# Performance work log

Hardware: AMD Instinct MI355X
Metric: run time of the kernel (lower is better)

The kernel has to match this reference:

```python
import jax, jax.numpy as jnp
import numpy as np

NF = 10      # num RBF / Chebyshev features
GAMMA = 1.0
EMB = 10
H = 64
NHEADS = 2


def _rbf(d):
    centers = jnp.arange(1, NF + 1, dtype=d.dtype)
    return jnp.exp(-GAMMA * (centers - d[..., None]) ** 2)


def _cheb(a):
    feats = [jnp.ones_like(a), a]
    for _ in range(2, NF):
        feats.append(2 * a * feats[-1] - feats[-2])
    return jnp.stack(feats, -1)


def _gru_layer(xs, wih, whh, bih, bhh):
    # xs: [L, B, D] -> [L, B, H]; PyTorch gate order r, z, n
    B = xs.shape[1]
    def step(h, xt):
        gi = xt @ wih.T + bih
        gh = h @ whh.T + bhh
        ir, iz, inn = jnp.split(gi, 3, -1)
        hr, hz, hn = jnp.split(gh, 3, -1)
        r = jax.nn.sigmoid(ir + hr)
        z = jax.nn.sigmoid(iz + hz)
        n = jnp.tanh(inn + r * hn)
        hnew = (1 - z) * n + z * h
        return hnew, hnew
    h0 = jnp.zeros((B, H), xs.dtype)
    _, ys = jax.lax.scan(step, h0, xs)
    return ys


def _mha(x, in_w, in_b, out_w, out_b):
    B, L, E = x.shape
    hd = E // NHEADS
    qkv = x @ in_w.T + in_b
    q, k, v = jnp.split(qkv, 3, -1)
    sp = lambda t: t.reshape(B, L, NHEADS, hd).transpose(0, 2, 1, 3)
    q, k, v = sp(q), sp(k), sp(v)
    scale = 1.0 / float(np.sqrt(hd))
    att = jax.nn.softmax(jnp.einsum('bhqd,bhkd->bhqk', q, k) * scale, -1)
    o = jnp.einsum('bhqk,bhkd->bhqd', att, v).transpose(0, 2, 1, 3).reshape(B, L, E)
    return o @ out_w.T + out_b


def _ln(x, s, b):
    m = x.mean(-1, keepdims=True)
    v = ((x - m) ** 2).mean(-1, keepdims=True)
    return (x - m) / jnp.sqrt(v + 1e-5) * s + b


def setup_inputs() -> dict:
    key = jax.random.key(0)
    ks = jax.random.split(key, 48)
    N, L = 384, 256
    # bond rows: [atom_idx1, atom_idx2, bond_dist]; angle rows: [d1, d2, angle]
    idx1 = jax.random.randint(ks[0], (N, L), 1, 119).astype(jnp.float32)
    idx2 = jax.random.randint(ks[1], (N, L), 1, 119).astype(jnp.float32)
    dist = jax.random.uniform(ks[2], (N, L), minval=0.5, maxval=5.0)
    d1 = jax.random.uniform(ks[3], (N, L), minval=0.5, maxval=5.0)
    d2 = jax.random.uniform(ks[4], (N, L), minval=0.5, maxval=5.0)
    ang = jax.random.uniform(ks[5], (N, L), minval=-1.0, maxval=1.0)
    bond_x = jnp.stack([idx1, idx2, dist], 1)
    angle_x = jnp.stack([d1, d2, ang], 1)
    is_angle = (jnp.arange(N) % 3 == 2)
    x = jnp.where(is_angle[:, None, None], angle_x, bond_x)

    def nrm(k, shp, s=0.1):
        return jax.random.normal(k, shp) * s

    D_IN = 2 * EMB + NF  # 30
    inp = {
        'x': x,
        'emb': nrm(ks[6], (119, EMB), 1.0),
        'wih0': nrm(ks[7], (3 * H, D_IN)),
        'whh0': nrm(ks[8], (3 * H, H)),
        'bih0': nrm(ks[9], (3 * H,)),
        'bhh0': nrm(ks[10], (3 * H,)),
        'wih12': nrm(ks[11], (2, 3 * H, H)),
        'whh12': nrm(ks[12], (2, 3 * H, H)),
        'bih12': nrm(ks[13], (2, 3 * H)),
        'bhh12': nrm(ks[14], (2, 3 * H)),
        'in_w1': nrm(ks[15], (3 * H, H)),
        'in_b1': nrm(ks[16], (3 * H,)),
        'out_w1': nrm(ks[17], (H, H)),
        'out_b1': nrm(ks[18], (H,)),
        'in_w2': nrm(ks[19], (3 * H, H)),
        'in_b2': nrm(ks[20], (3 * H,)),
        'out_w2': nrm(ks[21], (H, H)),
        'out_b2': nrm(ks[22], (H,)),
        'ff_w1': nrm(ks[23], (1024, H)),
        'ff_b1': nrm(ks[24], (1024,)),
        'ff_w2': nrm(ks[25], (H, 1024)),
        'ff_b2': nrm(ks[26], (H,)),
        'ln1_s': jnp.ones((H,)), 'ln1_b': jnp.zeros((H,)),
        'ln2_s': jnp.ones((H,)), 'ln2_b': jnp.zeros((H,)),
        'ln3_s': jnp.ones((H,)), 'ln3_b': jnp.zeros((H,)),
        'ln4_s': jnp.ones((H,)), 'ln4_b': jnp.zeros((H,)),
        'fw1': nrm(ks[27], (256, H)), 'fb1': nrm(ks[28], (256,)),
        'fw2': nrm(ks[29], (64, 256)), 'fb2': nrm(ks[30], (64,)),
        'fw3': nrm(ks[31], (32, 64)), 'fb3': nrm(ks[32], (32,)),
        'fw4': nrm(ks[33], (1, 32)), 'fb4': nrm(ks[34], (1,)),
    }
    return inp


def reference(x, emb, wih0, whh0, bih0, bhh0, wih12, whh12, bih12, bhh12,
              in_w1, in_b1, out_w1, out_b1, in_w2, in_b2, out_w2, out_b2,
              ff_w1, ff_b1, ff_w2, ff_b2,
              ln1_s, ln1_b, ln2_s, ln2_b, ln3_s, ln3_b, ln4_s, ln4_b,
              fw1, fb1, fw2, fb2, fw3, fb3, fw4, fb4):
    # Vectorized featurization (replaces the per-triplet Python loop):
    # rows with i%3 in {0,1} are bond rows, i%3==2 are angle rows.
    i1 = jnp.clip(x[:, 0].astype(jnp.int32), 0, 118)
    i2 = jnp.clip(x[:, 1].astype(jnp.int32), 0, 118)
    bond_feat = jnp.concatenate([emb[i1], emb[i2], _rbf(x[:, 2])], -1)
    angle_feat = jnp.concatenate([_rbf(x[:, 0]), _rbf(x[:, 1]), _cheb(x[:, 2])], -1)
    is_angle = (jnp.arange(x.shape[0]) % 3 == 2)
    feat = jnp.where(is_angle[:, None, None], angle_feat, bond_feat)  # [N, L, 30]

    hs = feat.transpose(1, 0, 2)  # [L, N, 30]
    hs = _gru_layer(hs, wih0, whh0, bih0, bhh0)
    for l in range(2):
        hs = _gru_layer(hs, wih12[l], whh12[l], bih12[l], bhh12[l])
    g = hs.transpose(1, 0, 2)  # [N, L, H]

    def ffn(t):
        return jax.nn.relu(jax.nn.relu(t @ ff_w1.T + ff_b1) @ ff_w2.T + ff_b2)

    a = _mha(g, in_w1, in_b1, out_w1, out_b1)
    h = _ln(g + a, ln1_s, ln1_b)
    h = _ln(h + ffn(h), ln2_s, ln2_b)
    a = _mha(h, in_w2, in_b2, out_w2, out_b2)
    h = _ln(a + a, ln3_s, ln3_b)  # faithful to original: attn_out + attn_out
    h = _ln(h + ffn(h), ln4_s, ln4_b)
    o = h[:, -1, :]
    o = jax.nn.silu(o @ fw1.T + fb1)
    o = jax.nn.silu(o @ fw2.T + fb2)
    o = jax.nn.silu(o @ fw3.T + fb3)
    o = o @ fw4.T + fb4
    return o.squeeze(-1)
```

## Files before the change

### kernel.cpp

```cpp
#include <hip/hip_runtime.h>

static constexpr int NB   = 384;
static constexpr int SEQL = 256;
static constexpr int NROWS = NB * SEQL;

typedef short bf16x8 __attribute__((ext_vector_type(8)));
typedef float f32x4  __attribute__((ext_vector_type(4)));

union B8u {
    bf16x8 v;
    ushort us[8];
    uint4  q;
};

__device__ inline ushort f2bf(float f) {
    uint u = __float_as_uint(f);
    uint r = u + 0x7FFFu + ((u >> 16) & 1u);
    return (ushort)(r >> 16);
}

__device__ inline void split8(float4 a, float4 b, B8u& hi, B8u& lo) {
    float f[8] = {a.x, a.y, a.z, a.w, b.x, b.y, b.z, b.w};
    #pragma unroll
    for (int i = 0; i < 8; ++i) {
        ushort h = f2bf(f[i]);
        hi.us[i] = h;
        float fh = __uint_as_float(((uint)h) << 16);
        lo.us[i] = f2bf(f[i] - fh);
    }
}

__global__ __launch_bounds__(256) void split_kernel(
    const float* __restrict__ src, ushort* __restrict__ hi,
    ushort* __restrict__ lo, int n)
{
    int i = blockIdx.x * 256 + threadIdx.x;
    if (i < n) {
        float f = src[i];
        ushort h = f2bf(f);
        hi[i] = h;
        float fh = __uint_as_float(((uint)h) << 16);
        lo[i] = f2bf(f - fh);
    }
}

__global__ __launch_bounds__(192) void featproj_kernel(
    const float* __restrict__ x, const float* __restrict__ emb,
    const float* __restrict__ wih0, const float* __restrict__ bih0,
    float* __restrict__ X)
{
    __shared__ float F[32][33];
    const int tid = threadIdx.x;
    const int m0  = blockIdx.x * 32;

    if (tid < 96) {
        const int r   = tid & 31;
        const int grp = tid >> 5;
        const int m   = m0 + r;
        const int b   = m % NB;
        const int l   = m / NB;
        const float* xb = x + (size_t)b * (3 * SEQL);
        const float x0 = xb[l], x1 = xb[SEQL + l], x2 = xb[2 * SEQL + l];
        const bool is_angle = (b % 3) == 2;
        float o[10];
        if (is_angle) {
            if (grp < 2) {
                const float a = (grp == 0) ? x0 : x1;
                #pragma unroll
                for (int c = 0; c < 10; ++c) { float d = (float)(c + 1) - a; o[c] = __expf(-d * d); }
            } else {
                float t0 = 1.f, t1 = x2;
                o[0] = 1.f; o[1] = x2;
                #pragma unroll
                for (int c = 2; c < 10; ++c) { float t = 2.f * x2 * t1 - t0; o[c] = t; t0 = t1; t1 = t; }
            }
        } else {
            if (grp < 2) {
                const float xv = (grp == 0) ? x0 : x1;
                int idx = (int)xv; idx = idx < 0 ? 0 : (idx > 118 ? 118 : idx);
                #pragma unroll
                for (int c = 0; c < 10; ++c) o[c] = emb[idx * 10 + c];
            } else {
                #pragma unroll
                for (int c = 0; c < 10; ++c) { float d = (float)(c + 1) - x2; o[c] = __expf(-d * d); }
            }
        }
        #pragma unroll
        for (int c = 0; c < 10; ++c) F[r][grp * 10 + c] = o[c];
    }
    __syncthreads();

    float w[30];
    #pragma unroll
    for (int k = 0; k < 30; ++k) w[k] = wih0[tid * 30 + k];
    const float bj = bih0[tid];
    for (int r = 0; r < 32; ++r) {
        float acc = bj;
        #pragma unroll
        for (int k = 0; k < 30; ++k) acc += F[r][k] * w[k];
        X[(size_t)(m0 + r) * 192 + tid] = acc;
    }
}

__global__ __launch_bounds__(192) void gru_kernel(
    const float* __restrict__ X, const float* __restrict__ whh,
    const float* __restrict__ bhh, float* __restrict__ Y, int out_batch_major)
{
    const int b = blockIdx.x;
    const int j = threadIdx.x;
    __shared__ float h[64];
    __shared__ float gis[192], ghs[192];

    float w[64];
    #pragma unroll
    for (int k = 0; k < 64; ++k) w[k] = whh[j * 64 + k];
    const float bj = bhh[j];
    if (j < 64) h[j] = 0.f;
    __syncthreads();

    for (int t = 0; t < SEQL; ++t) {
        const float gi = X[((size_t)t * NB + b) * 192 + j];
        float gh = bj;
        #pragma unroll
        for (int k = 0; k < 64; ++k) gh += h[k] * w[k];
        gis[j] = gi; ghs[j] = gh;
        __syncthreads();
        if (j < 64) {
            const float r = 1.f / (1.f + __expf(-(gis[j] + ghs[j])));
            const float z = 1.f / (1.f + __expf(-(gis[64 + j] + ghs[64 + j])));
            const float n = tanhf(gis[128 + j] + r * ghs[128 + j]);
            const float hn = (1.f - z) * n + z * h[j];
            h[j] = hn;
            const size_t row = out_batch_major ? ((size_t)b * SEQL + t)
                                               : ((size_t)t * NB + b);
            Y[row * 64 + j] = hn;
        }
        __syncthreads();
    }
}

template<int NCOLS>
__global__ __launch_bounds__(256, 2) void gemm_mfma(
    const float* __restrict__ A, const ushort* __restrict__ Whi,
    const ushort* __restrict__ Wlo, const float* __restrict__ bias,
    float* __restrict__ C)
{
    const int tid = threadIdx.x;
    const int w   = tid >> 6;
    const int lane = tid & 63;
    const int c = lane & 15;
    const int g = lane >> 4;
    const int m0 = blockIdx.x * 128 + 32 * w;

    B8u ah[2][2], al[2][2];
    #pragma unroll
    for (int rm = 0; rm < 2; ++rm) {
        const float* ap = A + (size_t)(m0 + 16 * rm + c) * 64;
        #pragma unroll
        for (int ks = 0; ks < 2; ++ks) {
            float4 v0 = *(const float4*)(ap + 32 * ks + 8 * g);
            float4 v1 = *(const float4*)(ap + 32 * ks + 8 * g + 4);
            split8(v0, v1, ah[rm][ks], al[rm][ks]);
        }
    }

    f32x4 acc[NCOLS / 16][2];
    #pragma unroll
    for (int nt = 0; nt < NCOLS / 16; ++nt) {
        float bv = bias[16 * nt + c];
        #pragma unroll
        for (int rm = 0; rm < 2; ++rm)
            acc[nt][rm] = (f32x4){bv, bv, bv, bv};
    }

    #pragma unroll
    for (int nt = 0; nt < NCOLS / 16; ++nt) {
        B8u wh[2], wl[2];
        #pragma unroll
        for (int ks = 0; ks < 2; ++ks) {
            size_t off = (size_t)(16 * nt + c) * 64 + 32 * ks + 8 * g;
            wh[ks].q = *(const uint4*)(Whi + off);
            wl[ks].q = *(const uint4*)(Wlo + off);
        }
        #pragma unroll
        for (int rm = 0; rm < 2; ++rm)
            #pragma unroll
            for (int ks = 0; ks < 2; ++ks) {
                acc[nt][rm] = __builtin_amdgcn_mfma_f32_16x16x32_bf16(ah[rm][ks].v, wh[ks].v, acc[nt][rm], 0, 0, 0);
                acc[nt][rm] = __builtin_amdgcn_mfma_f32_16x16x32_bf16(al[rm][ks].v, wh[ks].v, acc[nt][rm], 0, 0, 0);
                acc[nt][rm] = __builtin_amdgcn_mfma_f32_16x16x32_bf16(ah[rm][ks].v, wl[ks].v, acc[nt][rm], 0, 0, 0);
            }
    }

    #pragma unroll
    for (int nt = 0; nt < NCOLS / 16; ++nt)
        #pragma unroll
        for (int rm = 0; rm < 2; ++rm)
            #pragma unroll
            for (int reg = 0; reg < 4; ++reg) {
                int row = m0 + 16 * rm + 4 * g + reg;
                C[(size_t)row * NCOLS + 16 * nt + reg * 0 + c] = acc[nt][rm][reg];
            }
}

__global__ __launch_bounds__(256, 2) void ffn_mfma(
    const float* __restrict__ Xin,
    const ushort* __restrict__ W1hi, const ushort* __restrict__ W1lo,
    const ushort* __restrict__ W2hi, const ushort* __restrict__ W2lo,
    const float* __restrict__ b1, const float* __restrict__ b2,
    float* __restrict__ Out)
{
    __shared__ __align__(16) ushort sW1h[64 * 72], sW1l[64 * 72];
    __shared__ __align__(16) ushort sW2h[64 * 72], sW2l[64 * 72];
    __shared__ __align__(16) ushort sHh[128 * 72], sHl[128 * 72];
    __shared__ float sb1[64];

    const int tid = threadIdx.x;
    const int w   = tid >> 6;
    const int lane = tid & 63;
    const int c = lane & 15;
    const int g = lane >> 4;
    const int r0 = blockIdx.x * 128;

    B8u xh[2][2], xl[2][2];
    #pragma unroll
    for (int rm = 0; rm < 2; ++rm) {
        const float* ap = Xin + (size_t)(r0 + 32 * w + 16 * rm + c) * 64;
        #pragma unroll
        for (int ks = 0; ks < 2; ++ks) {
            float4 v0 = *(const float4*)(ap + 32 * ks + 8 * g);
            float4 v1 = *(const float4*)(ap + 32 * ks + 8 * g + 4);
            split8(v0, v1, xh[rm][ks], xl[rm][ks]);
        }
    }

    f32x4 acc2[4][2];
    #pragma unroll
    for (int jt = 0; jt < 4; ++jt) {
        float bv = b2[16 * jt + c];
        #pragma unroll
        for (int mt = 0; mt < 2; ++mt)
            acc2[jt][mt] = (f32x4){bv, bv, bv, bv};
    }

    for (int nc = 0; nc < 16; ++nc) {
        __syncthreads();
        {
            const int n = tid >> 2, s = tid & 3;
            size_t s1 = (size_t)(nc * 64 + n) * 64 + s * 16;
            size_t s2 = (size_t)n * 1024 + nc * 64 + s * 16;
            int d = n * 72 + s * 16;
            *(uint4*)&sW1h[d]     = *(const uint4*)(W1hi + s1);
            *(uint4*)&sW1h[d + 8] = *(const uint4*)(W1hi + s1 + 8);
            *(uint4*)&sW1l[d]     = *(const uint4*)(W1lo + s1);
            *(uint4*)&sW1l[d + 8] = *(const uint4*)(W1lo + s1 + 8);
            *(uint4*)&sW2h[d]     = *(const uint4*)(W2hi + s2);
            *(uint4*)&sW2h[d + 8] = *(const uint4*)(W2hi + s2 + 8);
            *(uint4*)&sW2l[d]     = *(const uint4*)(W2lo + s2);
            *(uint4*)&sW2l[d + 8] = *(const uint4*)(W2lo + s2 + 8);
            if (tid < 64) sb1[tid] = b1[nc * 64 + tid];
        }
        __syncthreads();

        f32x4 acc1[4][2];
        #pragma unroll
        for (int jm = 0; jm < 4; ++jm) {
            float b0 = sb1[16 * jm + 4 * g + 0];
            float b1v = sb1[16 * jm + 4 * g + 1];
            float b2v = sb1[16 * jm + 4 * g + 2];
            float b3v = sb1[16 * jm + 4 * g + 3];
            #pragma unroll
            for (int rm = 0; rm < 2; ++rm)
                acc1[jm][rm] = (f32x4){b0, b1v, b2v, b3v};
        }
        #pragma unroll
        for (int jm = 0; jm < 4; ++jm) {
            B8u w1h[2], w1l[2];
            #pragma unroll
            for (int ks = 0; ks < 2; ++ks) {
                int off = (16 * jm + c) * 72 + 32 * ks + 8 * g;
                w1h[ks].q = *(const uint4*)&sW1h[off];
                w1l[ks].q = *(const uint4*)&sW1l[off];
            }
            #pragma unroll
            for (int rm = 0; rm < 2; ++rm)
                #pragma unroll
                for (int ks = 0; ks < 2; ++ks) {
                    acc1[jm][rm] = __builtin_amdgcn_mfma_f32_16x16x32_bf16(w1h[ks].v, xh[rm][ks].v, acc1[jm][rm], 0, 0, 0);
                    acc1[jm][rm] = __builtin_amdgcn_mfma_f32_16x16x32_bf16(w1l[ks].v, xh[rm][ks].v, acc1[jm][rm], 0, 0, 0);
                    acc1[jm][rm] = __builtin_amdgcn_mfma_f32_16x16x32_bf16(w1h[ks].v, xl[rm][ks].v, acc1[jm][rm], 0, 0, 0);
                }
        }
        #pragma unroll
        for (int jm = 0; jm < 4; ++jm)
            #pragma unroll
            for (int rm = 0; rm < 2; ++rm) {
                ushort hh[4], hl[4];
                #pragma unroll
                for (int reg = 0; reg < 4; ++reg) {
                    float hv = fmaxf(acc1[jm][rm][reg], 0.f);
                    ushort h = f2bf(hv);
                    hh[reg] = h;
                    float fh = __uint_as_float(((uint)h) << 16);
                    hl[reg] = f2bf(hv - fh);
                }
                int el = (32 * w + 16 * rm + c) * 72 + 16 * jm + 4 * g;
                *(uint2*)&sHh[el] = make_uint2((uint)hh[0] | ((uint)hh[1] << 16),
                                               (uint)hh[2] | ((uint)hh[3] << 16));
                *(uint2*)&sHl[el] = make_uint2((uint)hl[0] | ((uint)hl[1] << 16),
                                               (uint)hl[2] | ((uint)hl[3] << 16));
            }
        asm volatile("s_waitcnt lgkmcnt(0)" ::: "memory");
        __builtin_amdgcn_sched_barrier(0);

        #pragma unroll
        for (int ks = 0; ks < 2; ++ks) {
            B8u ahh[2], ahl[2], bwh[4], bwl[4];
            #pragma unroll
            for (int mt = 0; mt < 2; ++mt) {
                int el = (32 * w + 16 * mt + c) * 72 + 32 * ks + 8 * g;
                ahh[mt].q = *(const uint4*)&sHh[el];
                ahl[mt].q = *(const uint4*)&sHl[el];
            }
            #pragma unroll
            for (int jt = 0; jt < 4; ++jt) {
                int el = (16 * jt + c) * 72 + 32 * ks + 8 * g;
                bwh[jt].q = *(const uint4*)&sW2h[el];
                bwl[jt].q = *(const uint4*)&sW2l[el];
            }
            #pragma unroll
            for (int jt = 0; jt < 4; ++jt)
                #pragma unroll
                for (int mt = 0; mt < 2; ++mt) {
                    acc2[jt][mt] = __builtin_amdgcn_mfma_f32_16x16x32_bf16(ahh[mt].v, bwh[jt].v, acc2[jt][mt], 0, 0, 0);
                    acc2[jt][mt] = __builtin_amdgcn_mfma_f32_16x16x32_bf16(ahl[mt].v, bwh[jt].v, acc2[jt][mt], 0, 0, 0);
                    acc2[jt][mt] = __builtin_amdgcn_mfma_f32_16x16x32_bf16(ahh[mt].v, bwl[jt].v, acc2[jt][mt], 0, 0, 0);
                }
        }
    }

    #pragma unroll
    for (int jt = 0; jt < 4; ++jt)
        #pragma unroll
        for (int mt = 0; mt < 2; ++mt)
            #pragma unroll
            for (int reg = 0; reg < 4; ++reg) {
                int row = r0 + 32 * w + 16 * mt + 4 * g + reg;
                Out[(size_t)row * 64 + 16 * jt + c] = fmaxf(acc2[jt][mt][reg], 0.f);
            }
}

__global__ __launch_bounds__(256, 2) void attn_mfma(
    const float* __restrict__ QKV, float* __restrict__ Out)
{
    __shared__ __align__(16) ushort Ph[4][4096];
    __shared__ __align__(16) ushort Pl[4][4096];

    const int h = blockIdx.x;
    const int b = blockIdx.y;
    const int tid = threadIdx.x;
    const int w = tid >> 6;
    const int lane = tid & 63;
    const int c = lane & 15;
    const int g = lane >> 4;
    const float scale = 0.17677669529663687f;

    const float* base = QKV + (size_t)b * SEQL * 192;
    ushort* phw = Ph[w];
    ushort* plw = Pl[w];

    B8u qh[4], ql[4];
    #pragma unroll
    for (int qt = 0; qt < 4; ++qt) {
        const float* p = base + (size_t)(64 * w + 16 * qt + c) * 192 + h * 32 + 8 * g;
        float4 v0 = *(const float4*)p;
        float4 v1 = *(const float4*)(p + 4);
        v0.x *= scale; v0.y *= scale; v0.z *= scale; v0.w *= scale;
        v1.x *= scale; v1.y *= scale; v1.z *= scale; v1.w *= scale;
        split8(v0, v1, qh[qt], ql[qt]);
    }

    f32x4 o[2][4];
    #pragma unroll
    for (int dt = 0; dt < 2; ++dt)
        #pragma unroll
        for (int qt = 0; qt < 4; ++qt)
            o[dt][qt] = (f32x4){0.f, 0.f, 0.f, 0.f};
    float mrun[4] = {-1e30f, -1e30f, -1e30f, -1e30f};
    float lrun[4] = {0.f, 0.f, 0.f, 0.f};

    for (int kc = 0; kc < 4; ++kc) {
        B8u kh[4], kl[4];
        #pragma unroll
        for (int kt = 0; kt < 4; ++kt) {
            const float* p = base + (size_t)(kc * 64 + 16 * kt + c) * 192 + 64 + h * 32 + 8 * g;
            split8(*(const float4*)p, *(const float4*)(p + 4), kh[kt], kl[kt]);
        }
        f32x4 st[4][4];
        #pragma unroll
        for (int kt = 0; kt < 4; ++kt)
            #pragma unroll
            for (int qt = 0; qt < 4; ++qt)
                st[kt][qt] = (f32x4){0.f, 0.f, 0.f, 0.f};
        #pragma unroll
        for (int kt = 0; kt < 4; ++kt)
            #pragma unroll
            for (int qt = 0; qt < 4; ++qt) {
                st[kt][qt] = __builtin_amdgcn_mfma_f32_16x16x32_bf16(kh[kt].v, qh[qt].v, st[kt][qt], 0, 0, 0);
                st[kt][qt] = __builtin_amdgcn_mfma_f32_16x16x32_bf16(kl[kt].v, qh[qt].v, st[kt][qt], 0, 0, 0);
                st[kt][qt] = __builtin_amdgcn_mfma_f32_16x16x32_bf16(kh[kt].v, ql[qt].v, st[kt][qt], 0, 0, 0);
            }

        asm volatile("s_waitcnt lgkmcnt(0)" ::: "memory");
        #pragma unroll
        for (int qt = 0; qt < 4; ++qt) {
            float cmax = st[0][qt][0];
            #pragma unroll
            for (int kt = 0; kt < 4; ++kt)
                #pragma unroll
                for (int r = 0; r < 4; ++r) cmax = fmaxf(cmax, st[kt][qt][r]);
            cmax = fmaxf(cmax, __shfl_xor(cmax, 16));
            cmax = fmaxf(cmax, __shfl_xor(cmax, 32));
            const float mnew = fmaxf(mrun[qt], cmax);
            const float corr = __expf(mrun[qt] - mnew);
            mrun[qt] = mnew;
            const int ql_ = 16 * qt + c;
            float csum = 0.f;
            #pragma unroll
            for (int kt = 0; kt < 4; ++kt) {
                ushort hh[4], hl[4];
                #pragma unroll
                for (int r = 0; r < 4; ++r) {
                    float pv = __expf(st[kt][qt][r] - mnew);
                    csum += pv;
                    ushort ph_ = f2bf(pv);
                    hh[r] = ph_;
                    hl[r] = f2bf(pv - __uint_as_float(((uint)ph_) << 16));
                }
                const int ow = (2 * kt + (g >> 1)) ^ (ql_ & 7);
                const int addr = ql_ * 64 + ow * 8 + (g & 1) * 4;
                *(uint2*)&phw[addr] = make_uint2((uint)hh[0] | ((uint)hh[1] << 16),
                                                 (uint)hh[2] | ((uint)hh[3] << 16));
                *(uint2*)&plw[addr] = make_uint2((uint)hl[0] | ((uint)hl[1] << 16),
                                                 (uint)hl[2] | ((uint)hl[3] << 16));
            }
            csum += __shfl_xor(csum, 16);
            csum += __shfl_xor(csum, 32);
            lrun[qt] = lrun[qt] * corr + csum;
            #pragma unroll
            for (int dt = 0; dt < 2; ++dt)
                #pragma unroll
                for (int r = 0; r < 4; ++r) o[dt][qt][r] *= corr;
        }

        B8u vh[2][2], vl[2][2];
        #pragma unroll
        for (int ks = 0; ks < 2; ++ks)
            #pragma unroll
            for (int dt = 0; dt < 2; ++dt) {
                const float* vp = base + (size_t)(kc * 64 + ks * 32 + 8 * g) * 192 + 128 + h * 32 + 16 * dt + c;
                float f0 = vp[0], f1 = vp[192], f2 = vp[384], f3 = vp[576];
                float f4 = vp[768], f5 = vp[960], f6 = vp[1152], f7 = vp[1344];
                split8(make_float4(f0, f1, f2, f3), make_float4(f4, f5, f6, f7),
                       vh[ks][dt], vl[ks][dt]);
            }

        asm volatile("s_waitcnt lgkmcnt(0)" ::: "memory");
        __builtin_amdgcn_sched_barrier(0);

        #pragma unroll
        for (int ks = 0; ks < 2; ++ks)
            #pragma unroll
            for (int qt = 0; qt < 4; ++qt) {
                const int ql_ = 16 * qt + c;
                const int orr = (ks * 4 + g) ^ (ql_ & 7);
                const int addr = ql_ * 64 + orr * 8;
                B8u pbh, pbl;
                pbh.q = *(const uint4*)&phw[addr];
                pbl.q = *(const uint4*)&plw[addr];
                #pragma unroll
                for (int dt = 0; dt < 2; ++dt) {
                    o[dt][qt] = __builtin_amdgcn_mfma_f32_16x16x32_bf16(vh[ks][dt].v, pbh.v, o[dt][qt], 0, 0, 0);
                    o[dt][qt] = __builtin_amdgcn_mfma_f32_16x16x32_bf16(vl[ks][dt].v, pbh.v, o[dt][qt], 0, 0, 0);
                    o[dt][qt] = __builtin_amdgcn_mfma_f32_16x16x32_bf16(vh[ks][dt].v, pbl.v, o[dt][qt], 0, 0, 0);
                }
            }
    }

    #pragma unroll
    for (int qt = 0; qt < 4; ++qt) {
        const float inv = 1.f / lrun[qt];
        const size_t row = (size_t)b * SEQL + 64 * w + 16 * qt + c;
        #pragma unroll
        for (int dt = 0; dt < 2; ++dt)
            #pragma unroll
            for (int r = 0; r < 4; ++r)
                Out[row * 64 + h * 32 + 16 * dt + 4 * g + r] = o[dt][qt][r] * inv;
    }
}

__global__ __launch_bounds__(256) void add_ln_kernel(
    const float* __restrict__ A, const float* __restrict__ B,
    const float* __restrict__ s, const float* __restrict__ bb,
    float* __restrict__ O)
{
    const size_t row = (size_t)blockIdx.x * 4 + (threadIdx.x >> 6);
    const int lane = threadIdx.x & 63;
    float v = A[row * 64 + lane] + B[row * 64 + lane];
    float sum = v;
    #pragma unroll
    for (int off = 32; off; off >>= 1) sum += __shfl_xor(sum, off);
    const float mean = sum * (1.f / 64.f);
    const float d = v - mean;
    float sq = d * d;
    #pragma unroll
    for (int off = 32; off; off >>= 1) sq += __shfl_xor(sq, off);
    const float var = sq * (1.f / 64.f);
    O[row * 64 + lane] = d * rsqrtf(var + 1e-5f) * s[lane] + bb[lane];
}

__global__ __launch_bounds__(256) void head_kernel(
    const float* __restrict__ Hf,
    const float* __restrict__ fw1, const float* __restrict__ fb1,
    const float* __restrict__ fw2, const float* __restrict__ fb2,
    const float* __restrict__ fw3, const float* __restrict__ fb3,
    const float* __restrict__ fw4, const float* __restrict__ fb4,
    float* __restrict__ out)
{
    const int b = blockIdx.x;
    const int tid = threadIdx.x;
    __shared__ float t0[64], t1[256], t2[64], t3[32];
    if (tid < 64) t0[tid] = Hf[((size_t)b * SEQL + (SEQL - 1)) * 64 + tid];
    __syncthreads();
    {
        float acc = fb1[tid];
        #pragma unroll 4
        for (int k = 0; k < 64; ++k) acc += t0[k] * fw1[tid * 64 + k];
        t1[tid] = acc / (1.f + __expf(-acc));
    }
    __syncthreads();
    if (tid < 64) {
        float acc = fb2[tid];
        #pragma unroll 4
        for (int k = 0; k < 256; ++k) acc += t1[k] * fw2[tid * 256 + k];
        t2[tid] = acc / (1.f + __expf(-acc));
    }
    __syncthreads();
    if (tid < 32) {
        float acc = fb3[tid];
        #pragma unroll 4
        for (int k = 0; k < 64; ++k) acc += t2[k] * fw3[tid * 64 + k];
        t3[tid] = acc / (1.f + __expf(-acc));
    }
    __syncthreads();
    if (tid == 0) {
        float acc = fb4[0];
        #pragma unroll
        for (int k = 0; k < 32; ++k) acc += t3[k] * fw4[k];
        out[b] = acc;
    }
}

extern "C" void kernel_launch(void* const* d_in, const int* in_sizes, int n_in,
                              void* d_out, int out_size, void* d_ws, size_t ws_size,
                              hipStream_t stream) {
    const float* x     = (const float*)d_in[0];
    const float* emb   = (const float*)d_in[1];
    const float* wih0  = (const float*)d_in[2];
    const float* whh0  = (const float*)d_in[3];
    const float* bih0  = (const float*)d_in[4];
    const float* bhh0  = (const float*)d_in[5];
    const float* wih12 = (const float*)d_in[6];
    const float* whh12 = (const float*)d_in[7];
    const float* bih12 = (const float*)d_in[8];
    const float* bhh12 = (const float*)d_in[9];
    const float* in_w1 = (const float*)d_in[10];
    const float* in_b1 = (const float*)d_in[11];
    const float* out_w1= (const float*)d_in[12];
    const float* out_b1= (const float*)d_in[13];
    const float* in_w2 = (const float*)d_in[14];
    const float* in_b2 = (const float*)d_in[15];
    const float* out_w2= (const float*)d_in[16];
    const float* out_b2= (const float*)d_in[17];
    const float* ff_w1 = (const float*)d_in[18];
    const float* ff_b1 = (const float*)d_in[19];
    const float* ff_w2 = (const float*)d_in[20];
    const float* ff_b2 = (const float*)d_in[21];
    const float* ln1_s = (const float*)d_in[22];
    const float* ln1_b = (const float*)d_in[23];
    const float* ln2_s = (const float*)d_in[24];
    const float* ln2_b = (const float*)d_in[25];
    const float* ln3_s = (const float*)d_in[26];
    const float* ln3_b = (const float*)d_in[27];
    const float* ln4_s = (const float*)d_in[28];
    const float* ln4_b = (const float*)d_in[29];
    const float* fw1   = (const float*)d_in[30];
    const float* fb1   = (const float*)d_in[31];
    const float* fw2   = (const float*)d_in[32];
    const float* fb2   = (const float*)d_in[33];
    const float* fw3   = (const float*)d_in[34];
    const float* fb3   = (const float*)d_in[35];
    const float* fw4   = (const float*)d_in[36];
    const float* fb4   = (const float*)d_in[37];

    float* ws = (float*)d_ws;
    float* X  = ws;
    float* S0 = X  + (size_t)NROWS * 192;
    float* S1 = S0 + (size_t)NROWS * 64;
    float* S2 = S1 + (size_t)NROWS * 64;

    ushort* bf = (ushort*)(S2 + (size_t)NROWS * 64);
    ushort* ffw1hi = bf;
    ushort* ffw1lo = ffw1hi + 65536;
    ushort* ffw2hi = ffw1lo + 65536;
    ushort* ffw2lo = ffw2hi + 65536;
    ushort* wghi   = ffw2lo + 65536;
    ushort* wglo   = wghi + 24576;
    ushort* q1hi   = wglo + 24576;
    ushort* q1lo   = q1hi + 12288;
    ushort* q2hi   = q1lo + 12288;
    ushort* q2lo   = q2hi + 12288;
    ushort* o1hi   = q2lo + 12288;
    ushort* o1lo   = o1hi + 4096;
    ushort* o2hi   = o1lo + 4096;
    ushort* o2lo   = o2hi + 4096;

    split_kernel<<<65536 / 256, 256, 0, stream>>>(ff_w1, ffw1hi, ffw1lo, 65536);
    split_kernel<<<65536 / 256, 256, 0, stream>>>(ff_w2, ffw2hi, ffw2lo, 65536);
    split_kernel<<<24576 / 256, 256, 0, stream>>>(wih12, wghi, wglo, 24576);
    split_kernel<<<12288 / 256, 256, 0, stream>>>(in_w1, q1hi, q1lo, 12288);
    split_kernel<<<12288 / 256, 256, 0, stream>>>(in_w2, q2hi, q2lo, 12288);
    split_kernel<<<4096 / 256, 256, 0, stream>>>(out_w1, o1hi, o1lo, 4096);
    split_kernel<<<4096 / 256, 256, 0, stream>>>(out_w2, o2hi, o2lo, 4096);

    featproj_kernel<<<NROWS / 32, 192, 0, stream>>>(x, emb, wih0, bih0, X);
    gru_kernel<<<NB, 192, 0, stream>>>(X, whh0, bhh0, S0, 0);
    gemm_mfma<192><<<NROWS / 128, 256, 0, stream>>>(S0, wghi, wglo, bih12, X);
    gru_kernel<<<NB, 192, 0, stream>>>(X, whh12, bhh12, S1, 0);
    gemm_mfma<192><<<NROWS / 128, 256, 0, stream>>>(S1, wghi + 12288, wglo + 12288, bih12 + 192, X);
    gru_kernel<<<NB, 192, 0, stream>>>(X, whh12 + 192 * 64, bhh12 + 192, S0, 1);

    gemm_mfma<192><<<NROWS / 128, 256, 0, stream>>>(S0, q1hi, q1lo, in_b1, X);
    attn_mfma<<<dim3(2, NB), 256, 0, stream>>>(X, S1);
    gemm_mfma<64><<<NROWS / 128, 256, 0, stream>>>(S1, o1hi, o1lo, out_b1, S2);
    add_ln_kernel<<<NROWS / 4, 256, 0, stream>>>(S0, S2, ln1_s, ln1_b, S1);
    ffn_mfma<<<NROWS / 128, 256, 0, stream>>>(S1, ffw1hi, ffw1lo, ffw2hi, ffw2lo, ff_b1, ff_b2, S2);
    add_ln_kernel<<<NROWS / 4, 256, 0, stream>>>(S1, S2, ln2_s, ln2_b, S0);

    gemm_mfma<192><<<NROWS / 128, 256, 0, stream>>>(S0, q2hi, q2lo, in_b2, X);
    attn_mfma<<<dim3(2, NB), 256, 0, stream>>>(X, S1);
    gemm_mfma<64><<<NROWS / 128, 256, 0, stream>>>(S1, o2hi, o2lo, out_b2, S2);
    add_ln_kernel<<<NROWS / 4, 256, 0, stream>>>(S2, S2, ln3_s, ln3_b, S1);
    ffn_mfma<<<NROWS / 128, 256, 0, stream>>>(S1, ffw1hi, ffw1lo, ffw2hi, ffw2lo, ff_b1, ff_b2, S2);
    add_ln_kernel<<<NROWS / 4, 256, 0, stream>>>(S1, S2, ln4_s, ln4_b, S0);

    head_kernel<<<NB, 256, 0, stream>>>(S0, fw1, fb1, fw2, fb2, fw3, fb3, fw4, fb4,
                                        (float*)d_out);
    (void)in_sizes; (void)n_in; (void)out_size; (void)ws_size;
}
```

Measured before the change: 1.057 ms.

## Restructure GRU recurrence to one wavefront per sequence without block barriers

The GRU kernel now runs 64 threads (a single wavefront) per batch element. Each thread holds the r, z and n weight rows for its hidden unit in registers, computes all three gates itself, and replaces __syncthreads with an LDS waitcnt plus a scheduling barrier. It also prefetches the next timestep's input projections, vectorises the h reads from LDS, and uses fast reciprocal and exp-based tanh. This removes the two block barriers and the shared-memory gate exchange per step, at the cost of about 192 weight registers per thread and a reliance on implicit wavefront lockstep for LDS ordering.

```diff
diff --git a/kernel.cpp b/kernel.cpp
--- a/kernel.cpp
+++ b/kernel.cpp
@@ -102,40 +102,69 @@
     }
 }
 
-__global__ __launch_bounds__(192) void gru_kernel(
+__global__ __launch_bounds__(64, 1) void gru_kernel(
     const float* __restrict__ X, const float* __restrict__ whh,
     const float* __restrict__ bhh, float* __restrict__ Y, int out_batch_major)
 {
     const int b = blockIdx.x;
     const int j = threadIdx.x;
     __shared__ float h[64];
-    __shared__ float gis[192], ghs[192];
-
-    float w[64];
-    #pragma unroll
-    for (int k = 0; k < 64; ++k) w[k] = whh[j * 64 + k];
-    const float bj = bhh[j];
-    if (j < 64) h[j] = 0.f;
-    __syncthreads();
+
+    float wr[64], wz[64], wn[64];
+    #pragma unroll
+    for (int k = 0; k < 16; ++k) {
+        float4 vr = *(const float4*)&whh[(size_t)(      j) * 64 + k * 4];
+        float4 vz = *(const float4*)&whh[(size_t)( 64 + j) * 64 + k * 4];
+        float4 vn = *(const float4*)&whh[(size_t)(128 + j) * 64 + k * 4];
+        wr[4*k+0] = vr.x; wr[4*k+1] = vr.y; wr[4*k+2] = vr.z; wr[4*k+3] = vr.w;
+        wz[4*k+0] = vz.x; wz[4*k+1] = vz.y; wz[4*k+2] = vz.z; wz[4*k+3] = vz.w;
+        wn[4*k+0] = vn.x; wn[4*k+1] = vn.y; wn[4*k+2] = vn.z; wn[4*k+3] = vn.w;
+    }
+    const float br = bhh[j], bz = bhh[64 + j], bn = bhh[128 + j];
+
+    float hj = 0.f;
+    h[j] = 0.f;
+    const float* x0p = X + (size_t)b * 192;
+    float gir = x0p[j], giz = x0p[64 + j], gin = x0p[128 + j];
+    asm volatile("s_waitcnt lgkmcnt(0)" ::: "memory");
+    __builtin_amdgcn_sched_barrier(0);
 
     for (int t = 0; t < SEQL; ++t) {
-        const float gi = X[((size_t)t * NB + b) * 192 + j];
-        float gh = bj;
-        #pragma unroll
-        for (int k = 0; k < 64; ++k) gh += h[k] * w[k];
-        gis[j] = gi; ghs[j] = gh;
-        __syncthreads();
-        if (j < 64) {
-            const float r = 1.f / (1.f + __expf(-(gis[j] + ghs[j])));
-            const float z = 1.f / (1.f + __expf(-(gis[64 + j] + ghs[64 + j])));
-            const float n = tanhf(gis[128 + j] + r * ghs[128 + j]);
-            const float hn = (1.f - z) * n + z * h[j];
-            h[j] = hn;
-            const size_t row = out_batch_major ? ((size_t)b * SEQL + t)
-                                               : ((size_t)t * NB + b);
-            Y[row * 64 + j] = hn;
-        }
-        __syncthreads();
+        const int tn = (t + 1 < SEQL) ? t + 1 : t;
+        const float* xp = X + ((size_t)tn * NB + b) * 192;
+        const float nr = xp[j], nz = xp[64 + j], nn = xp[128 + j];
+
+        float ar0 = br, ar1 = 0.f, az0 = bz, az1 = 0.f, an0 = bn, an1 = 0.f;
+        #pragma unroll
+        for (int k8 = 0; k8 < 8; ++k8) {
+            float4 h0 = *(const float4*)&h[k8 * 8];
+            float4 h1 = *(const float4*)&h[k8 * 8 + 4];
+            ar0 += h0.x*wr[k8*8+0] + h0.y*wr[k8*8+1] + h0.z*wr[k8*8+2] + h0.w*wr[k8*8+3];
+            ar1 += h1.x*wr[k8*8+4] + h1.y*wr[k8*8+5] + h1.z*wr[k8*8+6] + h1.w*wr[k8*8+7];
+            az0 += h0.x*wz[k8*8+0] + h0.y*wz[k8*8+1] + h0.z*wz[k8*8+2] + h0.w*wz[k8*8+3];
+            az1 += h1.x*wz[k8*8+4] + h1.y*wz[k8*8+5] + h1.z*wz[k8*8+6] + h1.w*wz[k8*8+7];
+            an0 += h0.x*wn[k8*8+0] + h0.y*wn[k8*8+1] + h0.z*wn[k8*8+2] + h0.w*wn[k8*8+3];
+            an1 += h1.x*wn[k8*8+4] + h1.y*wn[k8*8+5] + h1.z*wn[k8*8+6] + h1.w*wn[k8*8+7];
+        }
+        const float ghr = ar0 + ar1, ghz = az0 + az1, ghn = an0 + an1;
+
+        const float r = __builtin_amdgcn_rcpf(1.f + __expf(-(gir + ghr)));
+        const float z = __builtin_amdgcn_rcpf(1.f + __expf(-(giz + ghz)));
+        const float a = gin + r * ghn;
+        const float ea = __expf(-2.f * fabsf(a));
+        const float tn_ = (1.f - ea) * __builtin_amdgcn_rcpf(1.f + ea);
+        const float n = (a >= 0.f) ? tn_ : -tn_;
+        const float hn = (1.f - z) * n + z * hj;
+        hj = hn;
+
+        const size_t row = out_batch_major ? ((size_t)b * SEQL + t)
+                                           : ((size_t)t * NB + b);
+        Y[row * 64 + j] = hn;
+        gir = nr; giz = nz; gin = nn;
+
+        h[j] = hn;
+        asm volatile("s_waitcnt lgkmcnt(0)" ::: "memory");
+        __builtin_amdgcn_sched_barrier(0);
     }
 }
 
@@ -199,7 +228,7 @@
             #pragma unroll
             for (int reg = 0; reg < 4; ++reg) {
                 int row = m0 + 16 * rm + 4 * g + reg;
-                C[(size_t)row * NCOLS + 16 * nt + reg * 0 + c] = acc[nt][rm][reg];
+                C[(size_t)row * NCOLS + 16 * nt + c] = acc[nt][rm][reg];
             }
 }
 
@@ -634,11 +663,11 @@
     split_kernel<<<4096 / 256, 256, 0, stream>>>(out_w2, o2hi, o2lo, 4096);
 
     featproj_kernel<<<NROWS / 32, 192, 0, stream>>>(x, emb, wih0, bih0, X);
-    gru_kernel<<<NB, 192, 0, stream>>>(X, whh0, bhh0, S0, 0);
+    gru_kernel<<<NB, 64, 0, stream>>>(X, whh0, bhh0, S0, 0);
     gemm_mfma<192><<<NROWS / 128, 256, 0, stream>>>(S0, wghi, wglo, bih12, X);
-    gru_kernel<<<NB, 192, 0, stream>>>(X, whh12, bhh12, S1, 0);
+    gru_kernel<<<NB, 64, 0, stream>>>(X, whh12, bhh12, S1, 0);
     gemm_mfma<192><<<NROWS / 128, 256, 0, stream>>>(S1, wghi + 12288, wglo + 12288, bih12 + 192, X);
-    gru_kernel<<<NB, 192, 0, stream>>>(X, whh12 + 192 * 64, bhh12 + 192, S0, 1);
+    gru_kernel<<<NB, 64, 0, stream>>>(X, whh12 + 192 * 64, bhh12 + 192, S0, 1);
 
     gemm_mfma<192><<<NROWS / 128, 256, 0, stream>>>(S0, q1hi, q1lo, in_b1, X);
     attn_mfma<<<dim3(2, NB), 256, 0, stream>>>(X, S1);
```

Result: slower. 1.344 ms (+27.2%).

## Run GRU recurrence on MFMA with 16 sequences per block

Applied to the files above, without the earlier changes.

Replaces the scalar per-sequence GRU kernel (one block of 192 threads per batch element, each thread holding 64 weights and doing a dot product) with an MFMA kernel. Each block handles 16 batch elements, and the recurrent matmul uses split bf16 hi/lo 16x16x32 MFMAs with swizzled double-buffered LDS for the hidden state. The next step's input gates are prefetched to overlap global loads with compute. This cuts the serial per-step compute and sync cost, at the cost of bf16x3 precision emulation and only 24 blocks of parallelism.

```diff
diff --git a/kernel.cpp b/kernel.cpp
--- a/kernel.cpp
+++ b/kernel.cpp
@@ -12,6 +12,8 @@
     ushort us[8];
     uint4  q;
 };
+
+union F4u { float4 v; float f[4]; };
 
 __device__ inline ushort f2bf(float f) {
     uint u = __float_as_uint(f);
@@ -102,39 +104,121 @@
     }
 }
 
-__global__ __launch_bounds__(192) void gru_kernel(
-    const float* __restrict__ X, const float* __restrict__ whh,
-    const float* __restrict__ bhh, float* __restrict__ Y, int out_batch_major)
+__global__ __launch_bounds__(256, 1) void gru_mfma(
+    const float* __restrict__ X, const ushort* __restrict__ WhhHi,
+    const ushort* __restrict__ WhhLo, const float* __restrict__ bhh,
+    float* __restrict__ Y, int out_batch_major)
 {
-    const int b = blockIdx.x;
-    const int j = threadIdx.x;
-    __shared__ float h[64];
-    __shared__ float gis[192], ghs[192];
-
-    float w[64];
-    #pragma unroll
-    for (int k = 0; k < 64; ++k) w[k] = whh[j * 64 + k];
-    const float bj = bhh[j];
-    if (j < 64) h[j] = 0.f;
+    constexpr int PAD = 88;
+    __shared__ __align__(16) ushort Hh[2][16][PAD];
+    __shared__ __align__(16) ushort Hl[2][16][PAD];
+
+    const int tid  = threadIdx.x;
+    const int wt   = tid >> 6;
+    const int lane = tid & 63;
+    const int c    = lane & 15;
+    const int g    = lane >> 4;
+    const int b0   = blockIdx.x * 16;
+
+    B8u awh[3][2], awl[3][2];
+    #pragma unroll
+    for (int gam = 0; gam < 3; ++gam)
+        #pragma unroll
+        for (int ks = 0; ks < 2; ++ks) {
+            size_t off = (size_t)(64 * gam + 16 * wt + c) * 64 + 32 * ks + 8 * g;
+            awh[gam][ks].q = *(const uint4*)(WhhHi + off);
+            awl[gam][ks].q = *(const uint4*)(WhhLo + off);
+        }
+    float bg[3][4];
+    #pragma unroll
+    for (int gam = 0; gam < 3; ++gam)
+        #pragma unroll
+        for (int r = 0; r < 4; ++r)
+            bg[gam][r] = bhh[64 * gam + 16 * wt + 4 * g + r];
+
+    {
+        ushort* zh = &Hh[0][0][0];
+        ushort* zl = &Hl[0][0][0];
+        for (int i = tid; i < 2 * 16 * PAD; i += 256) { zh[i] = 0; zl[i] = 0; }
+    }
+    float hold[4] = {0.f, 0.f, 0.f, 0.f};
+
+    F4u gi[3];
+    {
+        const float* xp = X + ((size_t)(b0 + c)) * 192;
+        #pragma unroll
+        for (int gam = 0; gam < 3; ++gam)
+            gi[gam].v = *(const float4*)(xp + 64 * gam + 16 * wt + 4 * g);
+    }
     __syncthreads();
 
     for (int t = 0; t < SEQL; ++t) {
-        const float gi = X[((size_t)t * NB + b) * 192 + j];
-        float gh = bj;
-        #pragma unroll
-        for (int k = 0; k < 64; ++k) gh += h[k] * w[k];
-        gis[j] = gi; ghs[j] = gh;
-        __syncthreads();
-        if (j < 64) {
-            const float r = 1.f / (1.f + __expf(-(gis[j] + ghs[j])));
-            const float z = 1.f / (1.f + __expf(-(gis[64 + j] + ghs[64 + j])));
-            const float n = tanhf(gis[128 + j] + r * ghs[128 + j]);
-            const float hn = (1.f - z) * n + z * h[j];
-            h[j] = hn;
-            const size_t row = out_batch_major ? ((size_t)b * SEQL + t)
-                                               : ((size_t)t * NB + b);
-            Y[row * 64 + j] = hn;
-        }
+        const int p = t & 1;
+
+        B8u bh[2], bl[2];
+        #pragma unroll
+        for (int ks = 0; ks < 2; ++ks) {
+            const int sl = (4 * ks + g) ^ (c & 7);
+            bh[ks].q = *(const uint4*)&Hh[p][c][sl * 8];
+            bl[ks].q = *(const uint4*)&Hl[p][c][sl * 8];
+        }
+
+        f32x4 acc[3];
+        #pragma unroll
+        for (int gam = 0; gam < 3; ++gam)
+            acc[gam] = (f32x4){bg[gam][0], bg[gam][1], bg[gam][2], bg[gam][3]};
+        #pragma unroll
+        for (int gam = 0; gam < 3; ++gam)
+            #pragma unroll
+            for (int ks = 0; ks < 2; ++ks) {
+                acc[gam] = __builtin_amdgcn_mfma_f32_16x16x32_bf16(awh[gam][ks].v, bh[ks].v, acc[gam], 0, 0, 0);
+                acc[gam] = __builtin_amdgcn_mfma_f32_16x16x32_bf16(awl[gam][ks].v, bh[ks].v, acc[gam], 0, 0, 0);
+                acc[gam] = __builtin_amdgcn_mfma_f32_16x16x32_bf16(awh[gam][ks].v, bl[ks].v, acc[gam], 0, 0, 0);
+            }
+
+        F4u ngi[3];
+        {
+            const int tn = (t + 1 < SEQL) ? t + 1 : t;
+            const float* xp = X + ((size_t)tn * NB + b0 + c) * 192;
+            #pragma unroll
+            for (int gam = 0; gam < 3; ++gam)
+                ngi[gam].v = *(const float4*)(xp + 64 * gam + 16 * wt + 4 * g);
+        }
+
+        float hn4[4];
+        #pragma unroll
+        for (int r = 0; r < 4; ++r) {
+            const float rr = 1.f / (1.f + __expf(-(gi[0].f[r] + acc[0][r])));
+            const float zz = 1.f / (1.f + __expf(-(gi[1].f[r] + acc[1][r])));
+            const float nn = tanhf(gi[2].f[r] + rr * acc[2][r]);
+            hn4[r] = (1.f - zz) * nn + zz * hold[r];
+            hold[r] = hn4[r];
+        }
+
+        {
+            const size_t row = out_batch_major ? ((size_t)(b0 + c) * SEQL + t)
+                                               : ((size_t)t * NB + b0 + c);
+            *(float4*)&Y[row * 64 + 16 * wt + 4 * g] =
+                make_float4(hn4[0], hn4[1], hn4[2], hn4[3]);
+        }
+
+        {
+            ushort hh[4], hl[4];
+            #pragma unroll
+            for (int r = 0; r < 4; ++r) {
+                ushort h = f2bf(hn4[r]);
+                hh[r] = h;
+                hl[r] = f2bf(hn4[r] - __uint_as_float(((uint)h) << 16));
+            }
+            const int sl = (2 * wt + (g >> 1)) ^ (c & 7);
+            const int ad = sl * 8 + (g & 1) * 4;
+            *(uint2*)&Hh[p ^ 1][c][ad] = make_uint2((uint)hh[0] | ((uint)hh[1] << 16),
+                                                    (uint)hh[2] | ((uint)hh[3] << 16));
+            *(uint2*)&Hl[p ^ 1][c][ad] = make_uint2((uint)hl[0] | ((uint)hl[1] << 16),
+                                                    (uint)hl[2] | ((uint)hl[3] << 16));
+        }
+        #pragma unroll
+        for (int gam = 0; gam < 3; ++gam) gi[gam].v = ngi[gam].v;
         __syncthreads();
     }
 }
@@ -199,7 +283,7 @@
             #pragma unroll
             for (int reg = 0; reg < 4; ++reg) {
                 int row = m0 + 16 * rm + 4 * g + reg;
-                C[(size_t)row * NCOLS + 16 * nt + reg * 0 + c] = acc[nt][rm][reg];
+                C[(size_t)row * NCOLS + 16 * nt + c] = acc[nt][rm][reg];
             }
 }
 
@@ -624,6 +708,10 @@
     ushort* o1lo   = o1hi + 4096;
     ushort* o2hi   = o1lo + 4096;
     ushort* o2lo   = o2hi + 4096;
+    ushort* w0hi   = o2lo + 4096;
+    ushort* w0lo   = w0hi + 12288;
+    ushort* w12hi  = w0lo + 12288;
+    ushort* w12lo  = w12hi + 24576;
 
     split_kernel<<<65536 / 256, 256, 0, stream>>>(ff_w1, ffw1hi, ffw1lo, 65536);
     split_kernel<<<65536 / 256, 256, 0, stream>>>(ff_w2, ffw2hi, ffw2lo, 65536);
@@ -632,13 +720,15 @@
     split_kernel<<<12288 / 256, 256, 0, stream>>>(in_w2, q2hi, q2lo, 12288);
     split_kernel<<<4096 / 256, 256, 0, stream>>>(out_w1, o1hi, o1lo, 4096);
     split_kernel<<<4096 / 256, 256, 0, stream>>>(out_w2, o2hi, o2lo, 4096);
+    split_kernel<<<12288 / 256, 256, 0, stream>>>(whh0, w0hi, w0lo, 12288);
+    split_kernel<<<24576 / 256, 256, 0, stream>>>(whh12, w12hi, w12lo, 24576);
 
     featproj_kernel<<<NROWS / 32, 192, 0, stream>>>(x, emb, wih0, bih0, X);
-    gru_kernel<<<NB, 192, 0, stream>>>(X, whh0, bhh0, S0, 0);
+    gru_mfma<<<NB / 16, 256, 0, stream>>>(X, w0hi, w0lo, bhh0, S0, 0);
     gemm_mfma<192><<<NROWS / 128, 256, 0, stream>>>(S0, wghi, wglo, bih12, X);
-    gru_kernel<<<NB, 192, 0, stream>>>(X, whh12, bhh12, S1, 0);
+    gru_mfma<<<NB / 16, 256, 0, stream>>>(X, w12hi, w12lo, bhh12, S1, 0);
     gemm_mfma<192><<<NROWS / 128, 256, 0, stream>>>(S1, wghi + 12288, wglo + 12288, bih12 + 192, X);
-    gru_kernel<<<NB, 192, 0, stream>>>(X, whh12 + 192 * 64, bhh12 + 192, S0, 1);
+    gru_mfma<<<NB / 16, 256, 0, stream>>>(X, w12hi + 12288, w12lo + 12288, bhh12 + 192, S0, 1);
 
     gemm_mfma<192><<<NROWS / 128, 256, 0, stream>>>(S0, q1hi, q1lo, in_b1, X);
     attn_mfma<<<dim3(2, NB), 256, 0, stream>>>(X, S1);
```

New measurement: 1.253 ms (median of 2 runs). 1.19x slower.
